# Kernel optimization log

Hardware: AMD Instinct MI355X
Metric: run time of the kernel (lower is better)

The kernel has to match this reference:

```python
import jax, jax.numpy as jnp
import numpy as np

B, S, D = 2, 2048, 2048
H, HD = 16, 128          # n_heads, head_dim
RD = 64                  # rope_head_dim
ND = HD - RD             # nope_head_dim = 64
KVR, QR = 512, 1024      # kv_lora_rank, q_lora_rank
BASE = 10000.0
NEG = -1e30


def _apply_rope(t):
    # t: [B, H, S, RD]; GPT-NeoX half-split rotation
    half = RD // 2
    seq = t.shape[2]
    inv_freq = 1.0 / (BASE ** (jnp.arange(half, dtype=jnp.float32) / half))
    ang = jnp.arange(seq, dtype=jnp.float32)[:, None] * inv_freq  # [S, half]
    cos, sin = jnp.cos(ang), jnp.sin(ang)
    t1, t2 = t[..., :half], t[..., half:]
    return jnp.concatenate([t1 * cos - t2 * sin, t1 * sin + t2 * cos], axis=-1)


def setup_inputs() -> dict:
    key = jax.random.key(0)
    ks = jax.random.split(key, 9)
    def w(k, shape):  # weights stored [in, out], so y = x @ W
        return jax.random.normal(k, shape, jnp.float32) * (shape[0] ** -0.5)
    return {
        "x": jax.random.normal(ks[0], (B, S, D), jnp.float32),
        "Wq_down": w(ks[1], (D, QR)),
        "Wq_up": w(ks[2], (QR, H * ND)),
        "Wq_rope": w(ks[3], (QR, H * RD)),
        "Wkv_down": w(ks[4], (D, KVR)),
        "Wk_up": w(ks[5], (KVR, H * ND)),
        "Wk_rope": w(ks[6], (D, H * RD)),
        "Wv_up": w(ks[7], (KVR, H * HD)),
        "Wo": w(ks[8], (H * HD, D)),
    }


def reference(x, Wq_down, Wq_up, Wq_rope, Wkv_down, Wk_up, Wk_rope, Wv_up, Wo):
    b, s, _ = x.shape
    # low-rank query path
    q_lat = x @ Wq_down                                            # [B,S,QR]
    q_nope = (q_lat @ Wq_up).reshape(b, s, H, ND).transpose(0, 2, 1, 3)
    q_pe = (q_lat @ Wq_rope).reshape(b, s, H, RD).transpose(0, 2, 1, 3)
    # low-rank KV path (decoupled rope key comes straight from x)
    kv_lat = x @ Wkv_down                                          # [B,S,KVR]
    k_nope = (kv_lat @ Wk_up).reshape(b, s, H, ND).transpose(0, 2, 1, 3)
    k_pe = (x @ Wk_rope).reshape(b, s, H, RD).transpose(0, 2, 1, 3)
    v = (kv_lat @ Wv_up).reshape(b, s, H, HD).transpose(0, 2, 1, 3)
    # decoupled RoPE on the PE branches only
    q_pe = _apply_rope(q_pe)
    k_pe = _apply_rope(k_pe)
    q = jnp.concatenate([q_nope, q_pe], axis=-1)                   # [B,H,S,HD]
    k = jnp.concatenate([k_nope, k_pe], axis=-1)                   # [B,H,S,HD]
    # causal SDPA (no mask/cache supplied -> is_causal=True)
    scale = HD ** -0.5
    scores = jnp.einsum("bhqd,bhkd->bhqk", q, k) * scale
    causal = jnp.tril(jnp.ones((s, s), dtype=bool))
    scores = jnp.where(causal, scores, NEG)
    attn = jax.nn.softmax(scores, axis=-1)
    out = jnp.einsum("bhqk,bhkd->bhqd", attn, v)
    out = out.transpose(0, 2, 1, 3).reshape(b, s, H * HD)
    return out @ Wo
```

## Files before the change

### kernel.cpp

```cpp
#include <hip/hip_runtime.h>
#include <hip/hip_bf16.h>

typedef unsigned short u16;
typedef short bf16x8 __attribute__((ext_vector_type(8)));
typedef float f32x4 __attribute__((ext_vector_type(4)));

#define GLDS16(gp, lp) __builtin_amdgcn_global_load_lds( \
    (const __attribute__((address_space(1))) void*)(gp), \
    (__attribute__((address_space(3))) void*)(lp), 16, 0, 0)

static __device__ __forceinline__ u16 f2b(float f) {
  unsigned u = __float_as_uint(f);
  u += 0x7fffu + ((u >> 16) & 1u);
  return (u16)(u >> 16);
}
static __device__ __forceinline__ float b2f(u16 h) {
  return __uint_as_float(((unsigned)h) << 16);
}
static __device__ __forceinline__ f32x4 mfma16(bf16x8 a, bf16x8 b, f32x4 c) {
  return __builtin_amdgcn_mfma_f32_16x16x32_bf16(a, b, c, 0, 0, 0);
}
static __device__ __forceinline__ float fexp2(float x) {
  return __builtin_amdgcn_exp2f(x);
}

__device__ __align__(16) float g_rope[2048][64];

__global__ void rope_fill()
{
  int i = blockIdx.x * 256 + threadIdx.x;
  int s = i >> 5, j = i & 31;
  float invf = __expf(-(float)j * 0.28782313662425575f);
  float ang = (float)s * invf;
  g_rope[s][j] = cosf(ang);
  g_rope[s][32 + j] = sinf(ang);
}

__global__ void conv_f32_bf16(const float* __restrict__ src, u16* __restrict__ dst, int n4)
{
  int stride = gridDim.x * blockDim.x;
  for (int i = blockIdx.x * blockDim.x + threadIdx.x; i < n4; i += stride) {
    float4 v = ((const float4*)src)[i];
    ushort4 o;
    o.x = f2b(v.x); o.y = f2b(v.y); o.z = f2b(v.z); o.w = f2b(v.w);
    ((ushort4*)dst)[i] = o;
  }
}

__global__ void wtrans(const float* __restrict__ src, int K, int N,
                       u16* __restrict__ dst, int dld, int roff)
{
  __shared__ float tile[32][33];
  int n0 = blockIdx.x << 5, k0 = blockIdx.y << 5;
  int tx = threadIdx.x & 31, ty = threadIdx.x >> 5;
  #pragma unroll
  for (int p = 0; p < 4; ++p) {
    int kk = (p << 3) + ty;
    tile[kk][tx] = src[(size_t)(k0 + kk) * N + n0 + tx];
  }
  __syncthreads();
  #pragma unroll
  for (int p = 0; p < 4; ++p) {
    int nn = (p << 3) + ty;
    dst[(size_t)(roff + n0 + nn) * dld + k0 + tx] = f2b(tile[tx][nn]);
  }
}

__global__ __launch_bounds__(256, 2)
void gemm_bt(const u16* __restrict__ A, const u16* __restrict__ Bt,
             void* __restrict__ C, int K, int lda, int ldb, int ldc, int c_f32)
{
  __shared__ u16 As[2][128 * 64];
  __shared__ u16 Bs[2][128 * 64];
  const int t = threadIdx.x;
  const int lane = t & 63;
  const int m0 = blockIdx.y << 7, n0 = blockIdx.x << 7;
  const int w = t >> 6;
  const int wm = (w >> 1) << 6;
  const int wn = (w & 1) << 6;
  const int r15 = lane & 15, hi = lane >> 4;

  f32x4 acc[4][4];
  #pragma unroll
  for (int i = 0; i < 4; ++i)
    #pragma unroll
    for (int j = 0; j < 4; ++j)
      acc[i][j] = (f32x4){0.f, 0.f, 0.f, 0.f};

  auto STAGE = [&](int buf, int kt) {
    #pragma unroll
    for (int p = 0; p < 4; ++p) {
      int g = (p << 8) + t;
      int row = g >> 3;
      int sl = (g & 7) ^ (row & 7);
      const u16* ga = A + (size_t)(m0 + row) * lda + kt + (sl << 3);
      GLDS16(ga, (char*)As[buf] + g * 16);
      const u16* gb = Bt + (size_t)(n0 + row) * ldb + kt + (sl << 3);
      GLDS16(gb, (char*)Bs[buf] + g * 16);
    }
  };

  const int nk = K >> 6;
  STAGE(0, 0);
  __syncthreads();

  for (int ki = 0; ki < nk; ++ki) {
    int kn = (ki + 1 < nk) ? ki + 1 : ki;
    STAGE((ki + 1) & 1, kn << 6);
    const char* Ab = (const char*)As[ki & 1];
    const char* Bb = (const char*)Bs[ki & 1];
    #pragma unroll
    for (int kk = 0; kk < 2; ++kk) {
      int ks = (kk << 2) + hi;
      bf16x8 af[4], bfr[4];
      #pragma unroll
      for (int mi = 0; mi < 4; ++mi) {
        int row = wm + (mi << 4) + r15;
        af[mi] = *(const bf16x8*)(Ab + row * 128 + ((ks ^ (row & 7)) << 4));
      }
      #pragma unroll
      for (int ni = 0; ni < 4; ++ni) {
        int row = wn + (ni << 4) + r15;
        bfr[ni] = *(const bf16x8*)(Bb + row * 128 + ((ks ^ (row & 7)) << 4));
      }
      #pragma unroll
      for (int mi = 0; mi < 4; ++mi)
        #pragma unroll
        for (int ni = 0; ni < 4; ++ni)
          acc[mi][ni] = mfma16(af[mi], bfr[ni], acc[mi][ni]);
    }
    __syncthreads();
  }

  if (c_f32) {
    float* Cf = (float*)C;
    #pragma unroll
    for (int mi = 0; mi < 4; ++mi)
      #pragma unroll
      for (int ni = 0; ni < 4; ++ni) {
        int row = m0 + wm + (mi << 4) + (hi << 2);
        int col = n0 + wn + (ni << 4) + r15;
        #pragma unroll
        for (int r = 0; r < 4; ++r)
          Cf[(size_t)(row + r) * ldc + col] = acc[mi][ni][r];
      }
  } else {
    u16* Cb = (u16*)C;
    #pragma unroll
    for (int mi = 0; mi < 4; ++mi)
      #pragma unroll
      for (int ni = 0; ni < 4; ++ni) {
        int row = m0 + wm + (mi << 4) + (hi << 2);
        int col = n0 + wn + (ni << 4) + r15;
        #pragma unroll
        for (int r = 0; r < 4; ++r)
          Cb[(size_t)(row + r) * ldc + col] = f2b(acc[mi][ni][r]);
      }
  }
}

__global__ void pack_q(const u16* __restrict__ qout, u16* __restrict__ Qb)
{
  int rid = (blockIdx.x << 2) + (threadIdx.x >> 6);
  int lane = threadIdx.x & 63;
  int s = rid & 2047, h = (rid >> 11) & 15;
  int b = rid >> 15;
  const u16* src = qout + (size_t)((b << 11) + s) * 2048;
  const float scale = 0.12751743f;
  float vn = b2f(src[(h << 6) + lane]) * scale;
  int j = lane & 31;
  float t1 = b2f(src[1024 + (h << 6) + j]);
  float t2 = b2f(src[1024 + (h << 6) + 32 + j]);
  float c = g_rope[s][j], sn = g_rope[s][32 + j];
  float vp = (lane < 32) ? (t1 * c - t2 * sn) : (t1 * sn + t2 * c);
  vp *= scale;
  u16* dst = Qb + (size_t)rid * 128;
  dst[lane] = f2b(vn);
  dst[64 + lane] = f2b(vp);
}

__global__ void pack_k(const u16* __restrict__ kvout, const u16* __restrict__ lat1,
                       u16* __restrict__ Kb)
{
  int rid = (blockIdx.x << 2) + (threadIdx.x >> 6);
  int lane = threadIdx.x & 63;
  int s = rid & 2047, h = (rid >> 11) & 15;
  int b = rid >> 15;
  size_t row = (size_t)((b << 11) + s);
  float vn = b2f(kvout[row * 3072 + (h << 6) + lane]);
  int j = lane & 31;
  float t1 = b2f(lat1[row * 2560 + 1536 + (h << 6) + j]);
  float t2 = b2f(lat1[row * 2560 + 1536 + (h << 6) + 32 + j]);
  float c = g_rope[s][j], sn = g_rope[s][32 + j];
  float vp = (lane < 32) ? (t1 * c - t2 * sn) : (t1 * sn + t2 * c);
  u16* dst = Kb + (size_t)rid * 128;
  dst[lane] = f2b(vn);
  dst[64 + lane] = f2b(vp);
}

__global__ void pack_vt(const u16* __restrict__ kvout, u16* __restrict__ Vt)
{
  __shared__ u16 tile[32][33];
  int bi = blockIdx.x;
  int dt = bi & 3, st = (bi >> 2) & 63, h = (bi >> 8) & 15, b = bi >> 12;
  int tx = threadIdx.x & 31, ty = threadIdx.x >> 5;
  #pragma unroll
  for (int p = 0; p < 4; ++p) {
    int s = (st << 5) + (p << 3) + ty;
    tile[(p << 3) + ty][tx] =
        kvout[(size_t)((b << 11) + s) * 3072 + 1024 + (h << 7) + (dt << 5) + tx];
  }
  __syncthreads();
  #pragma unroll
  for (int p = 0; p < 4; ++p) {
    int d = (dt << 5) + (p << 3) + ty;
    Vt[(size_t)(((b << 4) + h) * 128 + d) * 2048 + (st << 5) + tx] = tile[tx][(p << 3) + ty];
  }
}

__global__ __launch_bounds__(512, 4)
void attn_fwd(const u16* __restrict__ Qb, const u16* __restrict__ Kb,
              const u16* __restrict__ Vt, u16* __restrict__ AO)
{
  __shared__ __align__(16) u16 Kl[2][64 * 128];
  __shared__ __align__(16) u16 Vl[128 * 64];
  __shared__ __align__(16) u16 Pl[8][16 * 64];

  const int S = 2048;
  int g = (int)(blockIdx.x >> 5);
  int qtg = (g < 8) ? (15 - g) : (g - 8);
  int bh = blockIdx.x & 31;
  int b = bh >> 4, h = bh & 15;
  int t = threadIdx.x, lane = t & 63, w = t >> 6;
  int q0 = qtg << 7;
  int qw = q0 + (w << 4);
  int r15 = lane & 15, hi = lane >> 4;

  const u16* Qp = Qb + (size_t)bh * S * 128;
  const u16* Kp = Kb + (size_t)bh * S * 128;
  const u16* Vp = Vt + (size_t)bh * 128 * S;

  bf16x8 qf[4];
  #pragma unroll
  for (int kk = 0; kk < 4; ++kk)
    qf[kk] = *(const bf16x8*)(Qp + (size_t)(qw + r15) * 128 + kk * 32 + hi * 8);

  f32x4 o[8];
  #pragma unroll
  for (int i = 0; i < 8; ++i) o[i] = (f32x4){0.f, 0.f, 0.f, 0.f};
  float mrun = -1e30f, lrun = 0.f;

  int qme = qw + r15;
  u16* pw = Pl[w];

  auto STAGE_K = [&](int buf, int kt) {
    #pragma unroll
    for (int p = 0; p < 2; ++p) {
      int gg = t + (p << 9);
      int rk = gg >> 4, ck = gg & 15, sk = ck ^ (rk & 15);
      const u16* ga = Kp + (size_t)((kt << 6) + rk) * 128 + (sk << 3);
      GLDS16(ga, (char*)Kl[buf] + gg * 16);
    }
  };
  auto STAGE_V = [&](int kt) {
    #pragma unroll
    for (int p = 0; p < 2; ++p) {
      int gg = t + (p << 9);
      int rv = gg >> 3, cv = gg & 7, sv = cv ^ (rv & 7);
      const u16* gv = Vp + (size_t)rv * S + (kt << 6) + (sv << 3);
      GLDS16(gv, (char*)Vl + gg * 16);
    }
  };

  const int ntiles = (qtg << 1) + 2;
  STAGE_K(0, 0);
  __syncthreads();

  for (int kt = 0; kt < ntiles; ++kt) {
    int kv0 = kt << 6;
    int ktn = (kt + 1 < ntiles) ? kt + 1 : kt;
    STAGE_V(kt);
    STAGE_K((kt + 1) & 1, ktn);

    bool part = (kv0 <= qw + 15);
    bf16x8 pf[2];
    if (part) {
      const char* Kcur = (const char*)Kl[kt & 1];
      f32x4 sc[4];
      __builtin_amdgcn_s_setprio(1);
      #pragma unroll
      for (int nt = 0; nt < 4; ++nt) {
        f32x4 a = (f32x4){0.f, 0.f, 0.f, 0.f};
        int row = (nt << 4) + r15;
        #pragma unroll
        for (int kk = 0; kk < 4; ++kk) {
          int ch = (kk << 2) + hi;
          bf16x8 kf = *(const bf16x8*)(Kcur + row * 256 + ((ch ^ (row & 15)) << 4));
          a = mfma16(kf, qf[kk], a);
        }
        sc[nt] = a;
      }
      __builtin_amdgcn_s_setprio(0);

      if (kv0 + 63 > qw) {
        #pragma unroll
        for (int nt = 0; nt < 4; ++nt) {
          int kvb = kv0 + (nt << 4) + (hi << 2);
          #pragma unroll
          for (int r = 0; r < 4; ++r)
            sc[nt][r] = (kvb + r <= qme) ? sc[nt][r] : -1e30f;
        }
      }

      f32x4 mx = sc[0];
      #pragma unroll
      for (int nt = 1; nt < 4; ++nt) {
        mx[0] = fmaxf(mx[0], sc[nt][0]); mx[1] = fmaxf(mx[1], sc[nt][1]);
        mx[2] = fmaxf(mx[2], sc[nt][2]); mx[3] = fmaxf(mx[3], sc[nt][3]);
      }
      float mt = fmaxf(fmaxf(mx[0], mx[1]), fmaxf(mx[2], mx[3]));
      mt = fmaxf(mt, __shfl_xor(mt, 16, 64));
      mt = fmaxf(mt, __shfl_xor(mt, 32, 64));
      float mn = fmaxf(mrun, mt);
      float cr = fexp2(mrun - mn);
      float ps = 0.f;
      #pragma unroll
      for (int nt = 0; nt < 4; ++nt) {
        #pragma unroll
        for (int r = 0; r < 4; ++r) {
          float pv = fexp2(sc[nt][r] - mn);
          sc[nt][r] = pv;
          ps += pv;
        }
      }
      ps += __shfl_xor(ps, 16, 64);
      ps += __shfl_xor(ps, 32, 64);
      lrun = lrun * cr + ps;
      mrun = mn;

      #pragma unroll
      for (int dt = 0; dt < 8; ++dt) {
        f32x4 t4 = o[dt];
        t4[0] *= cr; t4[1] *= cr; t4[2] *= cr; t4[3] *= cr;
        o[dt] = t4;
      }

      #pragma unroll
      for (int nt = 0; nt < 4; ++nt) {
        ushort4 pk;
        pk.x = f2b(sc[nt][0]); pk.y = f2b(sc[nt][1]);
        pk.z = f2b(sc[nt][2]); pk.w = f2b(sc[nt][3]);
        int chunk = ((nt << 1) + (hi >> 1)) ^ (r15 & 7);
        *(ushort4*)((char*)pw + r15 * 128 + (chunk << 4) + ((hi & 1) << 3)) = pk;
      }
      #pragma unroll
      for (int m = 0; m < 2; ++m) {
        int chunk = ((m << 2) + hi) ^ (r15 & 7);
        pf[m] = *(const bf16x8*)((const char*)pw + r15 * 128 + (chunk << 4));
      }
    }

    __syncthreads();

    if (part) {
      __builtin_amdgcn_s_setprio(1);
      #pragma unroll
      for (int dt = 0; dt < 8; ++dt) {
        int vrow = (dt << 4) + r15;
        #pragma unroll
        for (int m = 0; m < 2; ++m) {
          int chv = (m << 2) + hi;
          bf16x8 vf = *(const bf16x8*)((const char*)Vl + vrow * 128 + ((chv ^ (vrow & 7)) << 4));
          o[dt] = mfma16(vf, pf[m], o[dt]);
        }
      }
      __builtin_amdgcn_s_setprio(0);
    }

    __syncthreads();
  }

  float inv = 1.0f / lrun;
  size_t rowb = (size_t)(b * 2048 + qw + r15) * 2048 + h * 128 + (hi << 2);
  #pragma unroll
  for (int dt = 0; dt < 8; ++dt) {
    ushort4 ov;
    ov.x = f2b(o[dt][0] * inv); ov.y = f2b(o[dt][1] * inv);
    ov.z = f2b(o[dt][2] * inv); ov.w = f2b(o[dt][3] * inv);
    *(ushort4*)(AO + rowb + (dt << 4)) = ov;
  }
}

extern "C" void kernel_launch(void* const* d_in, const int* in_sizes, int n_in,
                              void* d_out, int out_size, void* d_ws, size_t ws_size,
                              hipStream_t stream)
{
  const float* x        = (const float*)d_in[0];
  const float* Wq_down  = (const float*)d_in[1];
  const float* Wq_up    = (const float*)d_in[2];
  const float* Wq_rope  = (const float*)d_in[3];
  const float* Wkv_down = (const float*)d_in[4];
  const float* Wk_up    = (const float*)d_in[5];
  const float* Wk_rope  = (const float*)d_in[6];
  const float* Wv_up    = (const float*)d_in[7];
  const float* Wo       = (const float*)d_in[8];

  char* ws = (char*)d_ws;
  u16* xb    = (u16*)(ws + 0);
  u16* W1t   = (u16*)(ws + 16777216);
  u16* W2t   = (u16*)(ws + 27262976);
  u16* W3t   = (u16*)(ws + 31457280);
  u16* Wot   = (u16*)(ws + 34603008);
  u16* lat1  = (u16*)(ws + 42991616);
  u16* qout  = (u16*)(ws + 63963136);
  u16* kvout = (u16*)(ws + 80740352);
  u16* Qb    = (u16*)(ws + 105906176);
  u16* Kb    = (u16*)(ws + 122683392);
  u16* Vtb   = (u16*)(ws + 139460608);
  u16* AO    = xb;
  if (ws_size < 156237824u) return;

  rope_fill<<<256, 256, 0, stream>>>();
  conv_f32_bf16<<<2048, 256, 0, stream>>>(x, xb, 2097152);

  wtrans<<<dim3(32, 64), 256, 0, stream>>>(Wq_down,  2048, 1024, W1t, 2048, 0);
  wtrans<<<dim3(16, 64), 256, 0, stream>>>(Wkv_down, 2048,  512, W1t, 2048, 1024);
  wtrans<<<dim3(32, 64), 256, 0, stream>>>(Wk_rope,  2048, 1024, W1t, 2048, 1536);
  wtrans<<<dim3(32, 32), 256, 0, stream>>>(Wq_up,    1024, 1024, W2t, 1024, 0);
  wtrans<<<dim3(32, 32), 256, 0, stream>>>(Wq_rope,  1024, 1024, W2t, 1024, 1024);
  wtrans<<<dim3(32, 16), 256, 0, stream>>>(Wk_up,     512, 1024, W3t,  512, 0);
  wtrans<<<dim3(64, 16), 256, 0, stream>>>(Wv_up,     512, 2048, W3t,  512, 1024);
  wtrans<<<dim3(64, 64), 256, 0, stream>>>(Wo,       2048, 2048, Wot, 2048, 0);

  gemm_bt<<<dim3(20, 32), 256, 0, stream>>>(xb, W1t, lat1, 2048, 2048, 2048, 2560, 0);
  gemm_bt<<<dim3(16, 32), 256, 0, stream>>>(lat1, W2t, qout, 1024, 2560, 1024, 2048, 0);
  gemm_bt<<<dim3(24, 32), 256, 0, stream>>>(lat1 + 1024, W3t, kvout, 512, 2560, 512, 3072, 0);

  pack_q<<<16384, 256, 0, stream>>>(qout, Qb);
  pack_k<<<16384, 256, 0, stream>>>(kvout, lat1, Kb);
  pack_vt<<<8192, 256, 0, stream>>>(kvout, Vtb);

  attn_fwd<<<512, 512, 0, stream>>>(Qb, Kb, Vtb, AO);

  gemm_bt<<<dim3(16, 32), 256, 0, stream>>>(AO, Wot, d_out, 2048, 2048, 2048, 2048, 1);

  (void)in_sizes; (void)n_in; (void)out_size;
}
```

Before: 436.5 us.

## Fuse Q/K/V packing and RoPE into GEMM epilogues, single-buffer GEMM LDS

Removes the pack_q, pack_k and pack_vt kernels and the qout/kvout intermediates. The GEMM epilogue now writes directly into the head-major Q/K layouts, applying the RoPE rotation and the query scale there, and writes V transposed. It also changes gemm_bt from double-buffered LDS staging to a single buffer with two barriers per k-step, which halves LDS use but removes the load/compute overlap. The scattered epilogue stores are less coalesced than the old row-major writes.

```diff
diff --git a/kernel.cpp b/kernel.cpp
--- a/kernel.cpp
+++ b/kernel.cpp
@@ -68,10 +68,11 @@
 
 __global__ __launch_bounds__(256, 2)
 void gemm_bt(const u16* __restrict__ A, const u16* __restrict__ Bt,
-             void* __restrict__ C, int K, int lda, int ldb, int ldc, int c_f32)
-{
-  __shared__ u16 As[2][128 * 64];
-  __shared__ u16 Bs[2][128 * 64];
+             void* __restrict__ C, int K, int lda, int ldb, int ldc,
+             int mode, u16* __restrict__ aux1, u16* __restrict__ aux2)
+{
+  __shared__ u16 As[128 * 64];
+  __shared__ u16 Bs[128 * 64];
   const int t = threadIdx.x;
   const int lane = t & 63;
   const int m0 = blockIdx.y << 7, n0 = blockIdx.x << 7;
@@ -87,28 +88,19 @@
     for (int j = 0; j < 4; ++j)
       acc[i][j] = (f32x4){0.f, 0.f, 0.f, 0.f};
 
-  auto STAGE = [&](int buf, int kt) {
+  for (int kt = 0; kt < K; kt += 64) {
+    __syncthreads();
     #pragma unroll
     for (int p = 0; p < 4; ++p) {
       int g = (p << 8) + t;
       int row = g >> 3;
       int sl = (g & 7) ^ (row & 7);
       const u16* ga = A + (size_t)(m0 + row) * lda + kt + (sl << 3);
-      GLDS16(ga, (char*)As[buf] + g * 16);
+      GLDS16(ga, (char*)As + g * 16);
       const u16* gb = Bt + (size_t)(n0 + row) * ldb + kt + (sl << 3);
-      GLDS16(gb, (char*)Bs[buf] + g * 16);
-    }
-  };
-
-  const int nk = K >> 6;
-  STAGE(0, 0);
-  __syncthreads();
-
-  for (int ki = 0; ki < nk; ++ki) {
-    int kn = (ki + 1 < nk) ? ki + 1 : ki;
-    STAGE((ki + 1) & 1, kn << 6);
-    const char* Ab = (const char*)As[ki & 1];
-    const char* Bb = (const char*)Bs[ki & 1];
+      GLDS16(gb, (char*)Bs + g * 16);
+    }
+    __syncthreads();
     #pragma unroll
     for (int kk = 0; kk < 2; ++kk) {
       int ks = (kk << 2) + hi;
@@ -116,12 +108,12 @@
       #pragma unroll
       for (int mi = 0; mi < 4; ++mi) {
         int row = wm + (mi << 4) + r15;
-        af[mi] = *(const bf16x8*)(Ab + row * 128 + ((ks ^ (row & 7)) << 4));
+        af[mi] = *(const bf16x8*)((const char*)As + row * 128 + ((ks ^ (row & 7)) << 4));
       }
       #pragma unroll
       for (int ni = 0; ni < 4; ++ni) {
         int row = wn + (ni << 4) + r15;
-        bfr[ni] = *(const bf16x8*)(Bb + row * 128 + ((ks ^ (row & 7)) << 4));
+        bfr[ni] = *(const bf16x8*)((const char*)Bs + row * 128 + ((ks ^ (row & 7)) << 4));
       }
       #pragma unroll
       for (int mi = 0; mi < 4; ++mi)
@@ -129,92 +121,98 @@
         for (int ni = 0; ni < 4; ++ni)
           acc[mi][ni] = mfma16(af[mi], bfr[ni], acc[mi][ni]);
     }
-    __syncthreads();
-  }
-
-  if (c_f32) {
+  }
+
+  const int row0 = m0 + wm + (hi << 2);
+
+  if (mode == 1) {
     float* Cf = (float*)C;
     #pragma unroll
     for (int mi = 0; mi < 4; ++mi)
       #pragma unroll
       for (int ni = 0; ni < 4; ++ni) {
-        int row = m0 + wm + (mi << 4) + (hi << 2);
+        int row = row0 + (mi << 4);
         int col = n0 + wn + (ni << 4) + r15;
         #pragma unroll
         for (int r = 0; r < 4; ++r)
           Cf[(size_t)(row + r) * ldc + col] = acc[mi][ni][r];
       }
-  } else {
+  } else if (mode == 0 || (mode == 2 && n0 < 1536)) {
     u16* Cb = (u16*)C;
     #pragma unroll
     for (int mi = 0; mi < 4; ++mi)
       #pragma unroll
       for (int ni = 0; ni < 4; ++ni) {
-        int row = m0 + wm + (mi << 4) + (hi << 2);
+        int row = row0 + (mi << 4);
         int col = n0 + wn + (ni << 4) + r15;
         #pragma unroll
         for (int r = 0; r < 4; ++r)
           Cb[(size_t)(row + r) * ldc + col] = f2b(acc[mi][ni][r]);
       }
-  }
-}
-
-__global__ void pack_q(const u16* __restrict__ qout, u16* __restrict__ Qb)
-{
-  int rid = (blockIdx.x << 2) + (threadIdx.x >> 6);
-  int lane = threadIdx.x & 63;
-  int s = rid & 2047, h = (rid >> 11) & 15;
-  int b = rid >> 15;
-  const u16* src = qout + (size_t)((b << 11) + s) * 2048;
-  const float scale = 0.12751743f;
-  float vn = b2f(src[(h << 6) + lane]) * scale;
-  int j = lane & 31;
-  float t1 = b2f(src[1024 + (h << 6) + j]);
-  float t2 = b2f(src[1024 + (h << 6) + 32 + j]);
-  float c = g_rope[s][j], sn = g_rope[s][32 + j];
-  float vp = (lane < 32) ? (t1 * c - t2 * sn) : (t1 * sn + t2 * c);
-  vp *= scale;
-  u16* dst = Qb + (size_t)rid * 128;
-  dst[lane] = f2b(vn);
-  dst[64 + lane] = f2b(vp);
-}
-
-__global__ void pack_k(const u16* __restrict__ kvout, const u16* __restrict__ lat1,
-                       u16* __restrict__ Kb)
-{
-  int rid = (blockIdx.x << 2) + (threadIdx.x >> 6);
-  int lane = threadIdx.x & 63;
-  int s = rid & 2047, h = (rid >> 11) & 15;
-  int b = rid >> 15;
-  size_t row = (size_t)((b << 11) + s);
-  float vn = b2f(kvout[row * 3072 + (h << 6) + lane]);
-  int j = lane & 31;
-  float t1 = b2f(lat1[row * 2560 + 1536 + (h << 6) + j]);
-  float t2 = b2f(lat1[row * 2560 + 1536 + (h << 6) + 32 + j]);
-  float c = g_rope[s][j], sn = g_rope[s][32 + j];
-  float vp = (lane < 32) ? (t1 * c - t2 * sn) : (t1 * sn + t2 * c);
-  u16* dst = Kb + (size_t)rid * 128;
-  dst[lane] = f2b(vn);
-  dst[64 + lane] = f2b(vp);
-}
-
-__global__ void pack_vt(const u16* __restrict__ kvout, u16* __restrict__ Vt)
-{
-  __shared__ u16 tile[32][33];
-  int bi = blockIdx.x;
-  int dt = bi & 3, st = (bi >> 2) & 63, h = (bi >> 8) & 15, b = bi >> 12;
-  int tx = threadIdx.x & 31, ty = threadIdx.x >> 5;
-  #pragma unroll
-  for (int p = 0; p < 4; ++p) {
-    int s = (st << 5) + (p << 3) + ty;
-    tile[(p << 3) + ty][tx] =
-        kvout[(size_t)((b << 11) + s) * 3072 + 1024 + (h << 7) + (dt << 5) + tx];
-  }
-  __syncthreads();
-  #pragma unroll
-  for (int p = 0; p < 4; ++p) {
-    int d = (dt << 5) + (p << 3) + ty;
-    Vt[(size_t)(((b << 4) + h) * 128 + d) * 2048 + (st << 5) + tx] = tile[tx][(p << 3) + ty];
+  } else if (mode == 3 && n0 < 1024) {
+    const float qs = 0.12751743f;
+    #pragma unroll
+    for (int mi = 0; mi < 4; ++mi)
+      #pragma unroll
+      for (int ni = 0; ni < 4; ++ni) {
+        int col = n0 + wn + (ni << 4) + r15;
+        int hh = col >> 6, d = col & 63;
+        #pragma unroll
+        for (int r = 0; r < 4; ++r) {
+          int row = row0 + (mi << 4) + r;
+          int b_ = row >> 11, s = row & 2047;
+          aux1[((size_t)(((b_ << 4) + hh) << 11) + s) * 128 + d] = f2b(acc[mi][ni][r] * qs);
+        }
+      }
+  } else if (mode == 4 && n0 < 1024) {
+    #pragma unroll
+    for (int mi = 0; mi < 4; ++mi)
+      #pragma unroll
+      for (int ni = 0; ni < 4; ++ni) {
+        int col = n0 + wn + (ni << 4) + r15;
+        int hh = col >> 6, d = col & 63;
+        #pragma unroll
+        for (int r = 0; r < 4; ++r) {
+          int row = row0 + (mi << 4) + r;
+          int b_ = row >> 11, s = row & 2047;
+          aux1[((size_t)(((b_ << 4) + hh) << 11) + s) * 128 + d] = f2b(acc[mi][ni][r]);
+        }
+      }
+  } else if (mode == 4) {
+    #pragma unroll
+    for (int mi = 0; mi < 4; ++mi)
+      #pragma unroll
+      for (int ni = 0; ni < 4; ++ni) {
+        int rel = (n0 - 1024) + wn + (ni << 4) + r15;
+        int hh = rel >> 7, d = rel & 127;
+        int row_s0 = row0 + (mi << 4);
+        int b_ = row_s0 >> 11, s0 = row_s0 & 2047;
+        ushort4 ov;
+        ov.x = f2b(acc[mi][ni][0]); ov.y = f2b(acc[mi][ni][1]);
+        ov.z = f2b(acc[mi][ni][2]); ov.w = f2b(acc[mi][ni][3]);
+        *(ushort4*)(aux2 + ((size_t)(((b_ << 4) + hh) << 7) + d) * 2048 + s0) = ov;
+      }
+  } else {
+    const int boff = (mode == 2) ? 1536 : 1024;
+    const float qs = (mode == 3) ? 0.12751743f : 1.0f;
+    #pragma unroll
+    for (int mi = 0; mi < 4; ++mi)
+      #pragma unroll
+      for (int ni = 0; ni < 2; ++ni) {
+        int rel = (n0 - boff) + wn + (ni << 4) + r15;
+        int hh = rel >> 6, j = rel & 31;
+        #pragma unroll
+        for (int r = 0; r < 4; ++r) {
+          int row = row0 + (mi << 4) + r;
+          int b_ = row >> 11, s = row & 2047;
+          float t1 = acc[mi][ni][r] * qs;
+          float t2 = acc[mi][ni | 2][r] * qs;
+          float c = g_rope[s][j], sn = g_rope[s][32 + j];
+          size_t base = ((size_t)(((b_ << 4) + hh) << 11) + s) * 128;
+          aux1[base + 64 + j] = f2b(t1 * c - t2 * sn);
+          aux1[base + 96 + j] = f2b(t1 * sn + t2 * c);
+        }
+      }
   }
 }
 
@@ -412,8 +410,6 @@
   u16* W3t   = (u16*)(ws + 31457280);
   u16* Wot   = (u16*)(ws + 34603008);
   u16* lat1  = (u16*)(ws + 42991616);
-  u16* qout  = (u16*)(ws + 63963136);
-  u16* kvout = (u16*)(ws + 80740352);
   u16* Qb    = (u16*)(ws + 105906176);
   u16* Kb    = (u16*)(ws + 122683392);
   u16* Vtb   = (u16*)(ws + 139460608);
@@ -432,17 +428,13 @@
   wtrans<<<dim3(64, 16), 256, 0, stream>>>(Wv_up,     512, 2048, W3t,  512, 1024);
   wtrans<<<dim3(64, 64), 256, 0, stream>>>(Wo,       2048, 2048, Wot, 2048, 0);
 
-  gemm_bt<<<dim3(20, 32), 256, 0, stream>>>(xb, W1t, lat1, 2048, 2048, 2048, 2560, 0);
-  gemm_bt<<<dim3(16, 32), 256, 0, stream>>>(lat1, W2t, qout, 1024, 2560, 1024, 2048, 0);
-  gemm_bt<<<dim3(24, 32), 256, 0, stream>>>(lat1 + 1024, W3t, kvout, 512, 2560, 512, 3072, 0);
-
-  pack_q<<<16384, 256, 0, stream>>>(qout, Qb);
-  pack_k<<<16384, 256, 0, stream>>>(kvout, lat1, Kb);
-  pack_vt<<<8192, 256, 0, stream>>>(kvout, Vtb);
+  gemm_bt<<<dim3(20, 32), 256, 0, stream>>>(xb, W1t, lat1, 2048, 2048, 2048, 2560, 2, Kb, nullptr);
+  gemm_bt<<<dim3(16, 32), 256, 0, stream>>>(lat1, W2t, Qb, 1024, 2560, 1024, 2048, 3, Qb, nullptr);
+  gemm_bt<<<dim3(24, 32), 256, 0, stream>>>(lat1 + 1024, W3t, Kb, 512, 2560, 512, 3072, 4, Kb, Vtb);
 
   attn_fwd<<<512, 512, 0, stream>>>(Qb, Kb, Vtb, AO);
 
-  gemm_bt<<<dim3(16, 32), 256, 0, stream>>>(AO, Wot, d_out, 2048, 2048, 2048, 2048, 1);
+  gemm_bt<<<dim3(16, 32), 256, 0, stream>>>(AO, Wot, d_out, 2048, 2048, 2048, 2048, 1, nullptr, nullptr);
 
   (void)in_sizes; (void)n_in; (void)out_size;
 }
```

New measurement: 366.2 us. 1.19x faster.
